# Kernel optimization log

Measured on AMD Instinct MI355X. Metric: run time of the kernel, lower is better.

The kernel has to match this reference:

```python
import jax, jax.numpy as jnp
import numpy as np

DIM = 512
HEADS = 8
DIM_HEAD = 64
HIDDEN = HEADS * DIM_HEAD  # 512
B = 4
L = 2048
SCALE = DIM_HEAD ** -0.5


def setup_inputs() -> dict:
    key = jax.random.key(0)
    k1, k2, k3, k4 = jax.random.split(key, 4)
    x = jax.random.normal(k1, (B, DIM, L), dtype=jnp.float32)
    # Conv1d with kernel_size=1 == pointwise matmul over channels; store as [out, in]
    w_qkv = jax.random.normal(k2, (HIDDEN * 3, DIM), dtype=jnp.float32) * (DIM ** -0.5)
    w_out = jax.random.normal(k3, (DIM, HIDDEN), dtype=jnp.float32) * (HIDDEN ** -0.5)
    b_out = jax.random.normal(k4, (DIM,), dtype=jnp.float32) * 0.01
    return {"x": x, "w_qkv": w_qkv, "w_out": w_out, "b_out": b_out}


def reference(x, w_qkv, w_out, b_out):
    # x: [B, dim, L]
    qkv = jnp.einsum('oi,bil->bol', w_qkv, x)           # [B, 3*hidden, L]
    q, k, v = jnp.split(qkv, 3, axis=1)                  # each [B, hidden, L]

    def to_heads(t):
        # 'b (h c) l -> b h l c'
        return t.reshape(t.shape[0], HEADS, DIM_HEAD, t.shape[-1]).transpose(0, 1, 3, 2)

    q = to_heads(q) * SCALE                              # [B, H, L, c]
    k = to_heads(k)
    v = to_heads(v)

    attn = jax.nn.softmax(jnp.einsum('bhqc,bhkc->bhqk', q, k), axis=-1)  # [B,H,L,L]
    o = jnp.einsum('bhqk,bhkc->bhqc', attn, v)           # [B, H, L, c]
    o = o.transpose(0, 1, 3, 2).reshape(o.shape[0], HIDDEN, o.shape[2] if False else L)
    # 'b h c l -> b (h c) l' done via transpose+reshape above
    out = jnp.einsum('oi,bil->bol', w_out, o) + b_out[None, :, None]
    return out
```

## Files before the change

kernel.cpp:

```cpp
#include <hip/hip_runtime.h>

typedef unsigned short u16;
typedef __bf16 bf16x8 __attribute__((ext_vector_type(8)));
typedef float f32x4 __attribute__((ext_vector_type(4)));

#define B_ 4
#define L_ 2048
#define LOG2E 1.44269504088896340736f
#define HSTRIDE ((size_t)L_ * 64)

__device__ __forceinline__ u16 f2bf(float f) {
    unsigned u = __float_as_uint(f);
    u += 0x7fff + ((u >> 16) & 1);
    return (u16)(u >> 16);
}

__device__ __forceinline__ unsigned pk2(float a, float b) {
    return __builtin_amdgcn_perm(__float_as_uint(b), __float_as_uint(a), 0x07060302u);
}

__device__ __forceinline__ f32x4 mfma16(bf16x8 a, bf16x8 b, f32x4 c) {
    return __builtin_amdgcn_mfma_f32_16x16x32_bf16(a, b, c, 0, 0, 0);
}

__device__ __forceinline__ void async16(const u16* g, u16* l) {
    __builtin_amdgcn_global_load_lds(
        (const __attribute__((address_space(1))) u16*)g,
        (__attribute__((address_space(3))) u16*)l, 16, 0, 0);
}

__global__ __launch_bounds__(256) void convert_f32_bf16(const float* __restrict__ in,
                                                        u16* __restrict__ out, int n) {
    int i = (blockIdx.x * 256 + threadIdx.x) * 4;
    if (i < n) {
        float4 f = *(const float4*)(in + i);
        ushort4 r;
        r.x = f2bf(f.x); r.y = f2bf(f.y); r.z = f2bf(f.z); r.w = f2bf(f.w);
        *(ushort4*)(out + i) = r;
    }
}

__global__ __launch_bounds__(256) void transpose_x(const float* __restrict__ x,
                                                   u16* __restrict__ xbt) {
    __shared__ u16 T[64][66];
    int b  = blockIdx.z;
    int i0 = blockIdx.y * 64;
    int l0 = blockIdx.x * 64;
    int t  = threadIdx.x;
    int c  = t & 63, r4 = t >> 6;
    const float* xb = x + ((size_t)b * 512 + i0) * 2048 + l0;
#pragma unroll
    for (int r = r4; r < 64; r += 4) T[r][c] = f2bf(xb[(size_t)r * 2048 + c]);
    __syncthreads();
    u16* ob = xbt + ((size_t)b * 2048 + l0) * 512 + i0;
#pragma unroll
    for (int r = r4; r < 64; r += 4) ob[(size_t)r * 512 + c] = T[c][r];
}

__global__ __launch_bounds__(256, 2) void qkv_gemm(const u16* __restrict__ xbt,
                                                   const u16* __restrict__ wq,
                                                   u16* __restrict__ qkv) {
    __shared__ u16 smem[16896];
    u16* As = smem;
    u16* Bs = smem + 8192;
    int b  = blockIdx.z;
    int m0 = blockIdx.x * 128;
    int n0 = blockIdx.y * 128;
    int tid = threadIdx.x;
    int lane = tid & 63, wid = tid >> 6;
    int quad = lane >> 4, n15 = lane & 15;
    const u16* Abase = xbt + ((size_t)b * L_ + m0) * 512;
    const u16* Bbase = wq + (size_t)n0 * 512;
    int mw = (wid & 1) * 64, nw = (wid >> 1) * 64;
    f32x4 acc[4][4] = {};
    for (int k0 = 0; k0 < 512; k0 += 64) {
        __syncthreads();
#pragma unroll
        for (int c = 0; c < 4; ++c) {
            int off = wid * 2048 + c * 512 + lane * 8;
            int row = off >> 6, col = off & 63;
            async16(Abase + (size_t)row * 512 + k0 + col, As + wid * 2048 + c * 512);
            async16(Bbase + (size_t)row * 512 + k0 + col, Bs + wid * 2048 + c * 512);
        }
        __syncthreads();
#pragma unroll
        for (int ks = 0; ks < 2; ++ks) {
            bf16x8 af[4], bfr[4];
#pragma unroll
            for (int i = 0; i < 4; ++i)
                af[i] = *(const bf16x8*)&As[(mw + i * 16 + n15) * 64 + ks * 32 + quad * 8];
#pragma unroll
            for (int j = 0; j < 4; ++j)
                bfr[j] = *(const bf16x8*)&Bs[(nw + j * 16 + n15) * 64 + ks * 32 + quad * 8];
#pragma unroll
            for (int i = 0; i < 4; ++i)
#pragma unroll
                for (int j = 0; j < 4; ++j)
                    acc[i][j] = mfma16(af[i], bfr[j], acc[i][j]);
        }
    }
    if (n0 < 1024) {
        __syncthreads();
        u16* T = smem;
        float sc = (n0 < 512) ? (0.125f * LOG2E) : 1.0f;
#pragma unroll
        for (int i = 0; i < 4; ++i)
#pragma unroll
            for (int j = 0; j < 4; ++j)
#pragma unroll
                for (int r = 0; r < 4; ++r)
                    T[(mw + i * 16 + quad * 4 + r) * 132 + (nw + j * 16 + n15)] =
                        f2bf(acc[i][j][r] * sc);
        __syncthreads();
        int t = (n0 < 512) ? 0 : 1;
        int h0 = (n0 >> 6) & 7;
        u16* plane = qkv + (((size_t)b * 3 + t) * 8 + h0) * HSTRIDE + (size_t)m0 * 64;
#pragma unroll
        for (int it = 0; it < 8; ++it) {
            int flat = it * 2048 + tid * 8;
            int h_loc = flat >> 13;
            int remh = flat & 8191;
            int src;
            if (t == 0) {
                int l_loc = remh >> 6, cc = remh & 63;
                src = l_loc * 132 + h_loc * 64 + cc;
            } else {
                int tile_loc = remh >> 10;
                int remt = remh & 1023;
                int ks_ = remt >> 9, qk = (remt >> 7) & 3, n15k = (remt >> 3) & 15;
                src = (tile_loc * 16 + n15k) * 132 + h_loc * 64 + ks_ * 32 + qk * 8;
            }
            ushort4 lo = *(const ushort4*)&T[src];
            ushort4 hi = *(const ushort4*)&T[src + 4];
            u16* dst = plane + (size_t)h_loc * HSTRIDE + remh;
            *(ushort4*)dst = lo;
            *(ushort4*)(dst + 4) = hi;
        }
    } else {
        int kt = m0 >> 7;
        u16* Vf = qkv + ((size_t)b * 3 + 2) * 8 * HSTRIDE;
#pragma unroll
        for (int i = 0; i < 4; ++i) {
            int L0 = mw + i * 16;
            int ks2 = (L0 >> 5) & 3;
            int r3 = ((L0 >> 3) + (quad >> 1)) & 3;
#pragma unroll
            for (int j = 0; j < 4; ++j) {
                int oo = (n0 - 1024) + nw + j * 16 + n15;
                int h = oo >> 6, c = oo & 63;
                ushort4 pk;
                pk.x = f2bf(acc[i][j][0]); pk.y = f2bf(acc[i][j][1]);
                pk.z = f2bf(acc[i][j][2]); pk.w = f2bf(acc[i][j][3]);
                *(ushort4*)&Vf[(size_t)h * HSTRIDE + kt * 8192 + ks2 * 2048
                               + (c >> 4) * 512 + r3 * 128 + n15 * 8 + (quad & 1) * 4] = pk;
            }
        }
    }
}

__global__ __launch_bounds__(256, 4) void attn_kernel(const u16* __restrict__ qkv,
                                                      u16* __restrict__ o2) {
    __shared__ u16 Ps[4 * 32 * 68];
    __shared__ float Ls[4][32];
    int bh = blockIdx.y;
    int b = bh >> 3, h = bh & 7;
    int q0 = blockIdx.x * 32;
    int tid = threadIdx.x, lane = tid & 63, wid = tid >> 6;
    int quad = lane >> 4, n15 = lane & 15;
    const u16* Qp = qkv + (((size_t)b * 3 + 0) * 8 + h) * HSTRIDE;
    const u16* Kf = qkv + (((size_t)b * 3 + 1) * 8 + h) * HSTRIDE;
    const u16* Vf = qkv + (((size_t)b * 3 + 2) * 8 + h) * HSTRIDE;
    u16* Pw = Ps + wid * (32 * 68);

    bf16x8 vones;
#pragma unroll
    for (int z = 0; z < 8; ++z) vones[z] = (__bf16)1.0f;

    bf16x8 aq[2][2];
#pragma unroll
    for (int mf = 0; mf < 2; ++mf)
#pragma unroll
        for (int ks = 0; ks < 2; ++ks)
            aq[mf][ks] = *(const bf16x8*)
                &Qp[(size_t)(q0 + mf * 16 + n15) * 64 + ks * 32 + quad * 8];

    f32x4 oacc[2][4] = {};
    f32x4 osum[2] = {};

    for (int it = 0; it < 8; ++it) {
        int tile0 = wid * 32 + it * 4;
#pragma unroll
        for (int nf = 0; nf < 4; ++nf) {
            const u16* kb = Kf + (size_t)(tile0 + nf) * 1024;
            bf16x8 ak0 = *(const bf16x8*)&kb[lane * 8];
            bf16x8 ak1 = *(const bf16x8*)&kb[512 + lane * 8];
#pragma unroll
            for (int mf = 0; mf < 2; ++mf) {
                f32x4 sT = {};
                sT = mfma16(ak0, aq[mf][0], sT);
                sT = mfma16(ak1, aq[mf][1], sT);
                float p0 = __builtin_amdgcn_exp2f(sT[0]);
                float p1 = __builtin_amdgcn_exp2f(sT[1]);
                float p2 = __builtin_amdgcn_exp2f(sT[2]);
                float p3 = __builtin_amdgcn_exp2f(sT[3]);
                uint2 pw;
                pw.x = pk2(p0, p1);
                pw.y = pk2(p2, p3);
                *(uint2*)&Pw[(mf * 16 + n15) * 68 + nf * 16 + quad * 4] = pw;
            }
        }
#pragma unroll
        for (int sub = 0; sub < 2; ++sub) {
            bf16x8 pa[2];
#pragma unroll
            for (int mf = 0; mf < 2; ++mf) {
                pa[mf] = *(const bf16x8*)&Pw[(mf * 16 + n15) * 68 + sub * 32 + quad * 8];
                osum[mf] = mfma16(pa[mf], vones, osum[mf]);
            }
            const u16* vbb = Vf + (size_t)(wid * 16 + it * 2 + sub) * 2048;
#pragma unroll
            for (int nf2 = 0; nf2 < 4; ++nf2) {
                bf16x8 vb = *(const bf16x8*)&vbb[nf2 * 512 + lane * 8];
#pragma unroll
                for (int mf = 0; mf < 2; ++mf)
                    oacc[mf][nf2] = mfma16(pa[mf], vb, oacc[mf][nf2]);
            }
        }
    }

#pragma unroll
    for (int mf = 0; mf < 2; ++mf)
#pragma unroll
        for (int r = 0; r < 4; ++r)
            Ls[wid][mf * 16 + quad * 4 + r] = osum[mf][r];
    float* Ored = (float*)Ps;
#pragma unroll
    for (int mf = 0; mf < 2; ++mf) {
        __syncthreads();
        float* Od = Ored + wid * (16 * 68);
#pragma unroll
        for (int nf2 = 0; nf2 < 4; ++nf2)
#pragma unroll
            for (int r = 0; r < 4; ++r)
                Od[(quad * 4 + r) * 68 + nf2 * 16 + n15] = oacc[mf][nf2][r];
        __syncthreads();
        int row = tid >> 4, c0 = (tid & 15) * 4;
        float4 a0 = *(float4*)&Ored[0 * 1088 + row * 68 + c0];
        float4 a1 = *(float4*)&Ored[1 * 1088 + row * 68 + c0];
        float4 a2 = *(float4*)&Ored[2 * 1088 + row * 68 + c0];
        float4 a3 = *(float4*)&Ored[3 * 1088 + row * 68 + c0];
        float inv = 1.0f / (Ls[0][mf * 16 + row] + Ls[1][mf * 16 + row]
                          + Ls[2][mf * 16 + row] + Ls[3][mf * 16 + row]);
        ushort4 ov;
        ov.x = f2bf((a0.x + a1.x + a2.x + a3.x) * inv);
        ov.y = f2bf((a0.y + a1.y + a2.y + a3.y) * inv);
        ov.z = f2bf((a0.z + a1.z + a2.z + a3.z) * inv);
        ov.w = f2bf((a0.w + a1.w + a2.w + a3.w) * inv);
        *(ushort4*)&o2[((size_t)b * L_ + q0 + mf * 16 + row) * 512 + h * 64 + c0] = ov;
    }
}

__global__ __launch_bounds__(256, 2) void out_gemm(const u16* __restrict__ wo,
                                                   const u16* __restrict__ o2,
                                                   const float* __restrict__ bout,
                                                   float* __restrict__ out) {
    __shared__ u16 As[4096], Bs[8192];
    int b  = blockIdx.z;
    int m0 = blockIdx.y * 64;
    int n0 = blockIdx.x * 128;
    int tid = threadIdx.x, lane = tid & 63, wid = tid >> 6;
    int quad = lane >> 4, n15 = lane & 15;
    const u16* Abase = wo + (size_t)m0 * 512;
    const u16* Bbase = o2 + ((size_t)b * L_ + n0) * 512;
    int mw = (wid & 1) * 32, nw = (wid >> 1) * 64;
    f32x4 acc[2][4] = {};
    for (int k0 = 0; k0 < 512; k0 += 64) {
        __syncthreads();
#pragma unroll
        for (int a = 0; a < 2; ++a) {
            int off = wid * 1024 + a * 512 + lane * 8;
            int row = off >> 6, col = off & 63;
            async16(Abase + (size_t)row * 512 + k0 + col, As + off);
        }
#pragma unroll
        for (int c = 0; c < 4; ++c) {
            int off = wid * 2048 + c * 512 + lane * 8;
            int row = off >> 6, col = off & 63;
            async16(Bbase + (size_t)row * 512 + k0 + col, Bs + off);
        }
        __syncthreads();
#pragma unroll
        for (int ks = 0; ks < 2; ++ks) {
            bf16x8 af[2], bfr[4];
#pragma unroll
            for (int i = 0; i < 2; ++i)
                af[i] = *(const bf16x8*)&As[(mw + i * 16 + n15) * 64 + ks * 32 + quad * 8];
#pragma unroll
            for (int j = 0; j < 4; ++j)
                bfr[j] = *(const bf16x8*)&Bs[(nw + j * 16 + n15) * 64 + ks * 32 + quad * 8];
#pragma unroll
            for (int i = 0; i < 2; ++i)
#pragma unroll
                for (int j = 0; j < 4; ++j)
                    acc[i][j] = mfma16(af[i], bfr[j], acc[i][j]);
        }
    }
#pragma unroll
    for (int i = 0; i < 2; ++i) {
#pragma unroll
        for (int r = 0; r < 4; ++r) {
            int o_ = m0 + mw + i * 16 + quad * 4 + r;
            float bias = bout[o_];
            float* dst = out + ((size_t)b * 512 + o_) * L_ + n0;
#pragma unroll
            for (int j = 0; j < 4; ++j) dst[nw + j * 16 + n15] = acc[i][j][r] + bias;
        }
    }
}

#define OFF_XBT  ((size_t)0)
#define OFF_WQKV (OFF_XBT + (size_t)B_ * L_ * 512)
#define OFF_WOUT (OFF_WQKV + (size_t)1536 * 512)
#define OFF_QKV  (OFF_WOUT + (size_t)512 * 512)
#define OFF_O2   (OFF_QKV + (size_t)3 * B_ * 8 * L_ * 64)

extern "C" void kernel_launch(void* const* d_in, const int* in_sizes, int n_in,
                              void* d_out, int out_size, void* d_ws, size_t ws_size,
                              hipStream_t stream) {
    (void)in_sizes; (void)n_in; (void)out_size; (void)ws_size;
    const float* x    = (const float*)d_in[0];
    const float* wqkv = (const float*)d_in[1];
    const float* wout = (const float*)d_in[2];
    const float* bout = (const float*)d_in[3];
    float* out = (float*)d_out;
    u16* ws = (u16*)d_ws;
    u16* xbt   = ws + OFF_XBT;
    u16* wqkvb = ws + OFF_WQKV;
    u16* woutb = ws + OFF_WOUT;
    u16* qkv   = ws + OFF_QKV;
    u16* o2    = ws + OFF_O2;

    convert_f32_bf16<<<768, 256, 0, stream>>>(wqkv, wqkvb, 1536 * 512);
    convert_f32_bf16<<<256, 256, 0, stream>>>(wout, woutb, 512 * 512);
    transpose_x<<<dim3(32, 8, 4), 256, 0, stream>>>(x, xbt);
    qkv_gemm<<<dim3(16, 12, 4), 256, 0, stream>>>(xbt, wqkvb, qkv);
    attn_kernel<<<dim3(64, 32), 256, 0, stream>>>(qkv, o2);
    out_gemm<<<dim3(16, 8, 4), 256, 0, stream>>>(woutb, o2, bout, out);
}
```

Before: 173.2 us.

## Merge prep kernels into one launch and software-prefetch K/V tiles in attention

The three preprocessing launches (two weight conversions and the x transpose) become a single kernel that picks its role from the block index, removing two kernel launches and their gaps. In the attention loop, the K and V fragments for the next iteration are loaded into registers while the current iteration's MFMAs run, and the loop is fully unrolled. This hides global-load latency behind compute, but it uses more registers, which may lower occupancy or cause spills.

New measurement: 161.0 us. -7.1%, faster.

```diff
diff --git a/kernel.cpp b/kernel.cpp
--- a/kernel.cpp
+++ b/kernel.cpp
@@ -29,32 +29,38 @@
         (__attribute__((address_space(3))) u16*)l, 16, 0, 0);
 }
 
-__global__ __launch_bounds__(256) void convert_f32_bf16(const float* __restrict__ in,
-                                                        u16* __restrict__ out, int n) {
-    int i = (blockIdx.x * 256 + threadIdx.x) * 4;
-    if (i < n) {
+__global__ __launch_bounds__(256) void prep_kernel(const float* __restrict__ x,
+                                                   const float* __restrict__ wqkv,
+                                                   const float* __restrict__ wout,
+                                                   u16* __restrict__ xbt,
+                                                   u16* __restrict__ wqkvb,
+                                                   u16* __restrict__ woutb) {
+    __shared__ u16 T[64][66];
+    int bid = blockIdx.x;
+    if (bid < 1024) {
+        const float* in = (bid < 768) ? wqkv : wout;
+        u16* out = (bid < 768) ? wqkvb : woutb;
+        int blk = (bid < 768) ? bid : (bid - 768);
+        int i = (blk * 256 + threadIdx.x) * 4;
         float4 f = *(const float4*)(in + i);
         ushort4 r;
         r.x = f2bf(f.x); r.y = f2bf(f.y); r.z = f2bf(f.z); r.w = f2bf(f.w);
         *(ushort4*)(out + i) = r;
-    }
-}
-
-__global__ __launch_bounds__(256) void transpose_x(const float* __restrict__ x,
-                                                   u16* __restrict__ xbt) {
-    __shared__ u16 T[64][66];
-    int b  = blockIdx.z;
-    int i0 = blockIdx.y * 64;
-    int l0 = blockIdx.x * 64;
-    int t  = threadIdx.x;
-    int c  = t & 63, r4 = t >> 6;
-    const float* xb = x + ((size_t)b * 512 + i0) * 2048 + l0;
-#pragma unroll
-    for (int r = r4; r < 64; r += 4) T[r][c] = f2bf(xb[(size_t)r * 2048 + c]);
-    __syncthreads();
-    u16* ob = xbt + ((size_t)b * 2048 + l0) * 512 + i0;
-#pragma unroll
-    for (int r = r4; r < 64; r += 4) ob[(size_t)r * 512 + c] = T[c][r];
+    } else {
+        int t0 = bid - 1024;
+        int b  = t0 >> 8;
+        int i0 = ((t0 >> 5) & 7) * 64;
+        int l0 = (t0 & 31) * 64;
+        int t  = threadIdx.x;
+        int c  = t & 63, r4 = t >> 6;
+        const float* xb = x + ((size_t)b * 512 + i0) * 2048 + l0;
+#pragma unroll
+        for (int r = r4; r < 64; r += 4) T[r][c] = f2bf(xb[(size_t)r * 2048 + c]);
+        __syncthreads();
+        u16* ob = xbt + ((size_t)b * 2048 + l0) * 512 + i0;
+#pragma unroll
+        for (int r = r4; r < 64; r += 4) ob[(size_t)r * 512 + c] = T[c][r];
+    }
 }
 
 __global__ __launch_bounds__(256, 2) void qkv_gemm(const u16* __restrict__ xbt,
@@ -187,18 +193,33 @@
     f32x4 oacc[2][4] = {};
     f32x4 osum[2] = {};
 
-    for (int it = 0; it < 8; ++it) {
-        int tile0 = wid * 32 + it * 4;
+    bf16x8 kf[4][2], vf[2][4];
+    {
+        int tile0 = wid * 32;
 #pragma unroll
         for (int nf = 0; nf < 4; ++nf) {
             const u16* kb = Kf + (size_t)(tile0 + nf) * 1024;
-            bf16x8 ak0 = *(const bf16x8*)&kb[lane * 8];
-            bf16x8 ak1 = *(const bf16x8*)&kb[512 + lane * 8];
+            kf[nf][0] = *(const bf16x8*)&kb[lane * 8];
+            kf[nf][1] = *(const bf16x8*)&kb[512 + lane * 8];
+        }
+#pragma unroll
+        for (int sub = 0; sub < 2; ++sub) {
+            const u16* vbb = Vf + (size_t)(wid * 16 + sub) * 2048;
+#pragma unroll
+            for (int nf2 = 0; nf2 < 4; ++nf2)
+                vf[sub][nf2] = *(const bf16x8*)&vbb[nf2 * 512 + lane * 8];
+        }
+    }
+
+#pragma unroll
+    for (int it = 0; it < 8; ++it) {
+#pragma unroll
+        for (int nf = 0; nf < 4; ++nf) {
 #pragma unroll
             for (int mf = 0; mf < 2; ++mf) {
                 f32x4 sT = {};
-                sT = mfma16(ak0, aq[mf][0], sT);
-                sT = mfma16(ak1, aq[mf][1], sT);
+                sT = mfma16(kf[nf][0], aq[mf][0], sT);
+                sT = mfma16(kf[nf][1], aq[mf][1], sT);
                 float p0 = __builtin_amdgcn_exp2f(sT[0]);
                 float p1 = __builtin_amdgcn_exp2f(sT[1]);
                 float p2 = __builtin_amdgcn_exp2f(sT[2]);
@@ -209,6 +230,15 @@
                 *(uint2*)&Pw[(mf * 16 + n15) * 68 + nf * 16 + quad * 4] = pw;
             }
         }
+        if (it < 7) {
+            int tile0 = wid * 32 + (it + 1) * 4;
+#pragma unroll
+            for (int nf = 0; nf < 4; ++nf) {
+                const u16* kb = Kf + (size_t)(tile0 + nf) * 1024;
+                kf[nf][0] = *(const bf16x8*)&kb[lane * 8];
+                kf[nf][1] = *(const bf16x8*)&kb[512 + lane * 8];
+            }
+        }
 #pragma unroll
         for (int sub = 0; sub < 2; ++sub) {
             bf16x8 pa[2];
@@ -217,13 +247,19 @@
                 pa[mf] = *(const bf16x8*)&Pw[(mf * 16 + n15) * 68 + sub * 32 + quad * 8];
                 osum[mf] = mfma16(pa[mf], vones, osum[mf]);
             }
-            const u16* vbb = Vf + (size_t)(wid * 16 + it * 2 + sub) * 2048;
-#pragma unroll
-            for (int nf2 = 0; nf2 < 4; ++nf2) {
-                bf16x8 vb = *(const bf16x8*)&vbb[nf2 * 512 + lane * 8];
+#pragma unroll
+            for (int nf2 = 0; nf2 < 4; ++nf2)
 #pragma unroll
                 for (int mf = 0; mf < 2; ++mf)
-                    oacc[mf][nf2] = mfma16(pa[mf], vb, oacc[mf][nf2]);
+                    oacc[mf][nf2] = mfma16(pa[mf], vf[sub][nf2], oacc[mf][nf2]);
+        }
+        if (it < 7) {
+#pragma unroll
+            for (int sub = 0; sub < 2; ++sub) {
+                const u16* vbb = Vf + (size_t)(wid * 16 + (it + 1) * 2 + sub) * 2048;
+#pragma unroll
+                for (int nf2 = 0; nf2 < 4; ++nf2)
+                    vf[sub][nf2] = *(const bf16x8*)&vbb[nf2 * 512 + lane * 8];
             }
         }
     }
@@ -340,9 +376,7 @@
     u16* qkv   = ws + OFF_QKV;
     u16* o2    = ws + OFF_O2;
 
-    convert_f32_bf16<<<768, 256, 0, stream>>>(wqkv, wqkvb, 1536 * 512);
-    convert_f32_bf16<<<256, 256, 0, stream>>>(wout, woutb, 512 * 512);
-    transpose_x<<<dim3(32, 8, 4), 256, 0, stream>>>(x, xbt);
+    prep_kernel<<<2048, 256, 0, stream>>>(x, wqkv, wout, xbt, wqkvb, woutb);
     qkv_gemm<<<dim3(16, 12, 4), 256, 0, stream>>>(xbt, wqkvb, qkv);
     attn_kernel<<<dim3(64, 32), 256, 0, stream>>>(qkv, o2);
     out_gemm<<<dim3(16, 8, 4), 256, 0, stream>>>(woutb, o2, bout, out);
```
